# Optimization experiments

Measured on AMD Instinct MI355X. Metric: run time of the kernel, lower is better.

Reference implementation:

```python
import jax, jax.numpy as jnp
import numpy as np
from jax import lax

N = 32768      # total nodes (8 graphs x 4096)
E = 262144     # edges (avg degree 8)
B = 8          # graphs in batch
TW = 25        # time window
H = 128        # hidden features
L = 6          # GNN layers
NV = 1         # n_variables (pos_t only)
SD = 1         # spatial dim
TMAX, TMIN, RES_T = 4.0, 0.0, 250.0
BD_LOW, BD_UP = 0.0, 16.0
EPS = 1e-5


def swish(x):
    return x * jax.nn.sigmoid(x)


def setup_inputs() -> dict:
    key = jax.random.key(0)
    ks = jax.random.split(key, 32)
    s = 0.05
    u = jax.random.normal(ks[0], (N, TW), jnp.float32)
    pos_t = jax.random.uniform(ks[1], (N, 1), jnp.float32) * TMAX
    pos_x = jax.random.uniform(ks[2], (N, 1), jnp.float32) * BD_UP
    pos = jnp.concatenate([pos_t, pos_x], axis=-1)
    edge_index = jax.random.randint(ks[3], (2, E), 0, N, jnp.int64)
    batch = jnp.repeat(jnp.arange(B, dtype=jnp.int64), N // B)
    d_in = TW + SD + NV          # 27
    d_msg = 2 * H + TW + SD + NV  # 282
    d_upd = H + H + NV            # 257
    We1 = jax.random.normal(ks[4], (d_in, H), jnp.float32) * s
    be1 = jnp.zeros((H,), jnp.float32)
    We2 = jax.random.normal(ks[5], (H, H), jnp.float32) * s
    be2 = jnp.zeros((H,), jnp.float32)
    Wm1 = jax.random.normal(ks[6], (L, d_msg, H), jnp.float32) * s
    bm1 = jnp.zeros((L, H), jnp.float32)
    Wm2 = jax.random.normal(ks[7], (L, H, H), jnp.float32) * s
    bm2 = jnp.zeros((L, H), jnp.float32)
    Wu1 = jax.random.normal(ks[8], (L, d_upd, H), jnp.float32) * s
    bu1 = jnp.zeros((L, H), jnp.float32)
    Wu2 = jax.random.normal(ks[9], (L, H, H), jnp.float32) * s
    bu2 = jnp.zeros((L, H), jnp.float32)
    Wc1 = jax.random.normal(ks[10], (8, 1, 16), jnp.float32) * s  # OIH
    bc1 = jnp.zeros((8,), jnp.float32)
    Wc2 = jax.random.normal(ks[11], (1, 8, 14), jnp.float32) * s
    bc2 = jnp.zeros((1,), jnp.float32)
    return dict(u=u, pos=pos, edge_index=edge_index, batch=batch,
                We1=We1, be1=be1, We2=We2, be2=be2,
                Wm1=Wm1, bm1=bm1, Wm2=Wm2, bm2=bm2,
                Wu1=Wu1, bu1=bu1, Wu2=Wu2, bu2=bu2,
                Wc1=Wc1, bc1=bc1, Wc2=Wc2, bc2=bc2)


def _mpnn(u, pos, edge_index, batch, We1, be1, We2, be2,
          Wm1, bm1, Wm2, bm2, Wu1, bu1, Wu2, bu2, Wc1, bc1, Wc2, bc2):
    src = edge_index[0]   # j (source)
    tgt = edge_index[1]   # i (target)
    pos_t = pos[:, 0:1] / TMAX
    pos_x = (pos[:, 1:] - BD_LOW) / (BD_UP - BD_LOW)
    variables = pos_t  # eq_variables empty -> only normalized time

    node_input = jnp.concatenate([u, pos_x, variables], axis=-1)  # [N, 27]
    h = swish(node_input @ We1 + be1)
    h = swish(h @ We2 + be2)

    # in-degree for scatter-mean (empty targets -> 0 like PyG mean)
    cnt = jnp.zeros((N,), jnp.float32).at[tgt].add(1.0)
    cnt = jnp.maximum(cnt, 1.0)[:, None]
    # per-graph node counts for InstanceNorm
    gcnt = jax.ops.segment_sum(jnp.ones((N,), jnp.float32), batch, num_segments=B)[:, None]

    u_diff_e = u[tgt] - u[src]          # [E, TW]
    p_diff_e = pos_x[tgt] - pos_x[src]  # [E, SD]
    var_i_e = variables[tgt]            # [E, NV]

    for l in range(L):
        # message: gather -> MLP per edge
        m_in = jnp.concatenate([h[tgt], h[src], u_diff_e, p_diff_e, var_i_e], axis=-1)  # [E, 282]
        msg = swish(m_in @ Wm1[l] + bm1[l])
        msg = swish(msg @ Wm2[l] + bm2[l])
        # scatter-mean aggregate onto targets
        agg = jax.ops.segment_sum(msg, tgt, num_segments=N) / cnt  # [N, H]
        # node update MLP, residual (in_features == out_features)
        up = jnp.concatenate([h, agg, variables], axis=-1)  # [N, 257]
        up = swish(up @ Wu1[l] + bu1[l])
        up = swish(up @ Wu2[l] + bu2[l])
        h = h + up
        # InstanceNorm per graph (no affine), biased variance
        mean = jax.ops.segment_sum(h, batch, num_segments=B) / gcnt      # [B, H]
        sq = jax.ops.segment_sum(h * h, batch, num_segments=B) / gcnt    # [B, H]
        var = sq - mean * mean
        h = (h - mean[batch]) / jnp.sqrt(var[batch] + EPS)

    # output CNN: tw=25 branch
    hc = h[:, None, :]  # [N, 1, 128]
    dn = ('NCH', 'OIH', 'NCH')
    c = lax.conv_general_dilated(hc, Wc1, (3,), 'VALID', dimension_numbers=dn) + bc1[None, :, None]
    c = swish(c)
    c = lax.conv_general_dilated(c, Wc2, (1,), 'VALID', dimension_numbers=dn) + bc2[None, :, None]
    diff = c[:, 0, :]  # [N, 25]

    dt = (TMAX - TMIN) / RES_T
    dt_cum = jnp.arange(1, TW + 1, dtype=jnp.float32) * dt  # cumsum of ones*dt
    out = u[:, -1:] + dt_cum[None, :] * diff
    return out


def reference(u, pos, edge_index, batch, We1, be1, We2, be2,
              Wm1, bm1, Wm2, bm2, Wu1, bu1, Wu2, bu2, Wc1, bc1, Wc2, bc2):
    return _mpnn(u, pos, edge_index, batch, We1, be1, We2, be2,
                 Wm1, bm1, Wm2, bm2, Wu1, bu1, Wu2, bu2, Wc1, bc1, Wc2, bc2)
```

## Files before the change

kernel.cpp:

```cpp
#include <hip/hip_runtime.h>
#include <stdint.h>

#define N_NODES 32768
#define N_EDGES 262144
#define NB 8
#define TW 25

typedef __attribute__((ext_vector_type(8))) short short8;
typedef __attribute__((ext_vector_type(4))) float floatx4;

#if defined(__has_builtin)
#if __has_builtin(__builtin_amdgcn_cvt_pk_bf16_f32)
#define HAVE_CVT_PK_BF16 1
#endif
#endif

__device__ __forceinline__ float swishf(float x) {
    return x * __builtin_amdgcn_rcpf(1.0f + __expf(-x));
}

__device__ __forceinline__ unsigned short f2bf(float x) {
    union { float f; unsigned u; } v; v.f = x;
    unsigned r = v.u + 0x7FFFu + ((v.u >> 16) & 1u);
    return (unsigned short)(r >> 16);
}
__device__ __forceinline__ unsigned pkbf(float a, float b) {
#ifdef HAVE_CVT_PK_BF16
    typedef __attribute__((ext_vector_type(2))) __bf16 bf16x2;
    union { bf16x2 v; unsigned u; } cv;
    cv.v = __builtin_amdgcn_cvt_pk_bf16_f32(a, b);
    return cv.u;
#else
    return (unsigned)f2bf(a) | ((unsigned)f2bf(b) << 16);
#endif
}
__device__ __forceinline__ float bf2f(unsigned short b) {
    union { unsigned u; float f; } v; v.u = ((unsigned)b) << 16; return v.f;
}

__global__ void init_kernel(const float* __restrict__ pos, const float* __restrict__ u,
                            float* __restrict__ posx, float* __restrict__ post,
                            unsigned short* __restrict__ feat) {
    int i = blockIdx.x * 256 + threadIdx.x;
    if (i < N_NODES) {
        float pt = pos[i * 2 + 0] * 0.25f;
        float px = pos[i * 2 + 1] * 0.0625f;
        post[i] = pt;
        posx[i] = px;
        unsigned short f[32];
        #pragma unroll
        for (int k = 0; k < 25; ++k) f[k] = f2bf(u[(size_t)i * 25 + k]);
        f[25] = f2bf(px);
        f[26] = f2bf(pt);
        #pragma unroll
        for (int k = 27; k < 32; ++k) f[k] = 0;
        #pragma unroll
        for (int j = 0; j < 4; ++j)
            *(uint4*)(feat + (size_t)i * 32 + j * 8) = *(uint4*)&f[j * 8];
    }
}

__global__ void deg_kernel(const int* __restrict__ tgt, int* __restrict__ deg) {
    int i = blockIdx.x * 256 + threadIdx.x;
    if (i < N_EDGES) atomicAdd(&deg[tgt[i]], 1);
}

__global__ __launch_bounds__(1024) void scan_kernel(const int* __restrict__ deg,
                                                    int* __restrict__ cursor) {
    __shared__ int ps[1024];
    int t = threadIdx.x;
    int base = t * 32;
    int tot = 0;
    for (int i = 0; i < 32; ++i) tot += deg[base + i];
    ps[t] = tot;
    __syncthreads();
    for (int off = 1; off < 1024; off <<= 1) {
        int v = (t >= off) ? ps[t - off] : 0;
        __syncthreads();
        ps[t] += v;
        __syncthreads();
    }
    int run = ps[t] - tot;
    for (int i = 0; i < 32; ++i) {
        cursor[base + i] = run;
        run += deg[base + i];
    }
}

__global__ void scatter_kernel(const int* __restrict__ src, const int* __restrict__ tgt,
                               int* __restrict__ cursor,
                               int* __restrict__ src_s, int* __restrict__ tgt_s) {
    int i = blockIdx.x * 256 + threadIdx.x;
    if (i < N_EDGES) {
        int tg = tgt[i];
        int p = atomicAdd(&cursor[tg], 1);
        src_s[p] = src[i];
        tgt_s[p] = tg;
    }
}

__global__ __launch_bounds__(256) void pack_kernel(const float* __restrict__ W,
                                                   unsigned short* __restrict__ Wp,
                                                   int Kreal, int Kc, int total) {
    int id = blockIdx.x * 256 + threadIdx.x;
    if (id >= total) return;
    int lane = id & 63;
    int t8 = (id >> 6) & 7;
    int rest = id >> 9;
    int c = rest % Kc;
    int l = rest / Kc;
    int n = t8 * 16 + (lane & 15);
    int kb = c * 32 + (lane >> 4) * 8;
    short8 v;
    #pragma unroll
    for (int j = 0; j < 8; ++j) {
        int k = kb + j;
        float x = (k < Kreal) ? W[((size_t)l * Kreal + k) * 128 + n] : 0.f;
        v[j] = (short)f2bf(x);
    }
    *(short8*)(Wp + (size_t)id * 8) = v;
}

__global__ __launch_bounds__(256) void pack_cat_kernel(const float* __restrict__ Wm1,
                                                       unsigned short* __restrict__ Wp) {
    int id = blockIdx.x * 256 + threadIdx.x;
    if (id >= 30720) return;
    int lane = id & 63;
    int tile = (id >> 6) & 15;
    int rest = id >> 10;
    int c = rest % 5;
    int l = rest / 5;
    int n = tile * 16 + (lane & 15);
    int col = n & 127;
    bool isT = n < 128;
    int kb = c * 32 + (lane >> 4) * 8;
    const float* W = Wm1 + (size_t)l * 283 * 128;
    short8 v;
    #pragma unroll
    for (int j = 0; j < 8; ++j) {
        int k = kb + j;
        float x = 0.f;
        if (k < 128) {
            x = W[(size_t)(isT ? k : 128 + k) * 128 + col];
        } else if (k < 155) {
            int row = 256 + (k - 128);
            x = W[(size_t)row * 128 + col];
            if (!isT) x = (row == 282) ? 0.f : -x;
        }
        v[j] = (short)f2bf(x);
    }
    *(short8*)(Wp + (size_t)id * 8) = v;
}

__global__ __launch_bounds__(256) void encoder_kernel(
    const float* __restrict__ u, const float* __restrict__ posx,
    const float* __restrict__ post,
    const float* __restrict__ We1, const float* __restrict__ be1,
    const float* __restrict__ We2, const float* __restrict__ be2,
    unsigned short* __restrict__ hraw, float* __restrict__ agg)
{
    __shared__ __align__(16) float As_[64 * 36];
    __shared__ __align__(16) float Ws[32 * 128];
    __shared__ __align__(16) float Ms[64 * 128];

    int t = threadIdx.x;
    int n0 = blockIdx.x * 64;
    int rg = t >> 5, cg = t & 31;

    {
        int r = t & 63, cseg = t >> 6;
        float4 z = make_float4(0.f, 0.f, 0.f, 0.f);
        #pragma unroll
        for (int j = 0; j < 8; ++j)
            *(float4*)(agg + (size_t)(n0 + r) * 128 + cseg * 32 + j * 4) = z;
    }

    float acc[8][4] = {};
    {
        int kk = t >> 3, cb = (t & 7) * 16;
        #pragma unroll
        for (int j = 0; j < 4; ++j) {
            float4 w = make_float4(0.f, 0.f, 0.f, 0.f);
            if (kk < 27) w = *(const float4*)&We1[kk * 128 + cb + j * 4];
            *(float4*)&Ws[kk * 128 + cb + j * 4] = w;
        }
        int el = t >> 2, kb = (t & 3) * 8, n = n0 + el;
        float v[8];
        #pragma unroll
        for (int j = 0; j < 8; ++j) {
            int k = kb + j;
            float x = 0.f;
            if (k < 25) x = u[n * 25 + k];
            else if (k == 25) x = posx[n];
            else if (k == 26) x = post[n];
            v[j] = x;
        }
        #pragma unroll
        for (int j = 0; j < 8; j += 4)
            *(float4*)&As_[el * 36 + kb + j] = make_float4(v[j], v[j+1], v[j+2], v[j+3]);
        __syncthreads();
        #pragma unroll 4
        for (int kk2 = 0; kk2 < 32; ++kk2) {
            float4 b = *(const float4*)&Ws[kk2 * 128 + cg * 4];
            float a[8];
            #pragma unroll
            for (int i = 0; i < 8; ++i) a[i] = As_[(rg * 8 + i) * 36 + kk2];
            #pragma unroll
            for (int i = 0; i < 8; ++i) {
                acc[i][0] += a[i] * b.x; acc[i][1] += a[i] * b.y;
                acc[i][2] += a[i] * b.z; acc[i][3] += a[i] * b.w;
            }
        }
        __syncthreads();
    }
    {
        float4 b1 = *(const float4*)&be1[cg * 4];
        #pragma unroll
        for (int i = 0; i < 8; ++i) {
            float4 m;
            m.x = swishf(acc[i][0] + b1.x);
            m.y = swishf(acc[i][1] + b1.y);
            m.z = swishf(acc[i][2] + b1.z);
            m.w = swishf(acc[i][3] + b1.w);
            *(float4*)&Ms[(rg * 8 + i) * 128 + cg * 4] = m;
        }
        __syncthreads();
    }
    float acc2[8][4] = {};
    for (int k0 = 0; k0 < 128; k0 += 32) {
        int kk = t >> 3, cb = (t & 7) * 16;
        #pragma unroll
        for (int j = 0; j < 4; ++j)
            *(float4*)&Ws[kk * 128 + cb + j * 4] =
                *(const float4*)&We2[(k0 + kk) * 128 + cb + j * 4];
        __syncthreads();
        #pragma unroll 4
        for (int kk2 = 0; kk2 < 32; ++kk2) {
            float4 b = *(const float4*)&Ws[kk2 * 128 + cg * 4];
            float a[8];
            #pragma unroll
            for (int i = 0; i < 8; ++i) a[i] = Ms[(rg * 8 + i) * 128 + (k0 + kk2)];
            #pragma unroll
            for (int i = 0; i < 8; ++i) {
                acc2[i][0] += a[i] * b.x; acc2[i][1] += a[i] * b.y;
                acc2[i][2] += a[i] * b.z; acc2[i][3] += a[i] * b.w;
            }
        }
        __syncthreads();
    }
    {
        float4 b2 = *(const float4*)&be2[cg * 4];
        #pragma unroll
        for (int i = 0; i < 8; ++i) {
            int n = n0 + rg * 8 + i;
            float4 o;
            o.x = swishf(acc2[i][0] + b2.x);
            o.y = swishf(acc2[i][1] + b2.y);
            o.z = swishf(acc2[i][2] + b2.z);
            o.w = swishf(acc2[i][3] + b2.w);
            uint2 pk;
            pk.x = pkbf(o.x, o.y);
            pk.y = pkbf(o.z, o.w);
            *(uint2*)(hraw + (size_t)n * 128 + cg * 4) = pk;
        }
    }
}

__global__ __launch_bounds__(512, 4) void premsg_kernel(
    const unsigned short* __restrict__ hraw,
    const float* __restrict__ stats, int donorm,
    const unsigned short* __restrict__ feat,
    const unsigned short* __restrict__ Wp, const float* __restrict__ b1,
    unsigned short* __restrict__ h_bf,
    float* __restrict__ At, float* __restrict__ As)
{
    __shared__ __align__(16) unsigned short A[64 * 168];
    __shared__ float mean_s[128];
    __shared__ float rstd_s[128];

    int t = threadIdx.x;
    int n0 = blockIdx.x * 64;
    int bidx = n0 >> 12;

    if (t < 128) {
        float mn = 0.f, rs = 1.f;
        if (donorm) {
            float s1 = stats[bidx * 128 + t] * (1.f / 4096.f);
            float s2 = stats[(NB + bidx) * 128 + t] * (1.f / 4096.f);
            mn = s1;
            rs = rsqrtf(s2 - s1 * s1 + 1e-5f);
        }
        mean_s[t] = mn;
        rstd_s[t] = rs;
    }
    __syncthreads();

    {
        int r = t & 63, cseg = t >> 6;
        int n = n0 + r;
        uint4 raw0 = *(const uint4*)(hraw + (size_t)n * 128 + cseg * 16);
        uint4 raw1 = *(const uint4*)(hraw + (size_t)n * 128 + cseg * 16 + 8);
        unsigned pk[8];
        #pragma unroll
        for (int j = 0; j < 8; ++j) {
            unsigned word = (j < 4) ? ((const unsigned*)&raw0)[j]
                                    : ((const unsigned*)&raw1)[j - 4];
            int c0 = cseg * 16 + j * 2;
            float v0 = (bf2f((unsigned short)(word & 0xffffu)) - mean_s[c0]) * rstd_s[c0];
            float v1 = (bf2f((unsigned short)(word >> 16)) - mean_s[c0 + 1]) * rstd_s[c0 + 1];
            pk[j] = pkbf(v0, v1);
        }
        *(uint4*)(A + r * 168 + cseg * 16)     = *(uint4*)&pk[0];
        *(uint4*)(A + r * 168 + cseg * 16 + 8) = *(uint4*)&pk[4];
        *(uint4*)(h_bf + (size_t)n * 128 + cseg * 16)     = *(uint4*)&pk[0];
        *(uint4*)(h_bf + (size_t)n * 128 + cseg * 16 + 8) = *(uint4*)&pk[4];
        if (cseg < 2) {
            uint4 f0 = *(const uint4*)(feat + (size_t)n * 32 + cseg * 16);
            uint4 f1 = *(const uint4*)(feat + (size_t)n * 32 + cseg * 16 + 8);
            *(uint4*)(A + r * 168 + 128 + cseg * 16)     = f0;
            *(uint4*)(A + r * 168 + 128 + cseg * 16 + 8) = f1;
        }
    }
    __syncthreads();

    int w = t >> 6, lane = t & 63, q = lane >> 4, m = lane & 15;
    floatx4 accT[4] = {};
    floatx4 accS[4] = {};
    #pragma unroll
    for (int c = 0; c < 5; ++c) {
        short8 bT = *(const short8*)(Wp + ((size_t)(c * 16 + w) * 64 + lane) * 8);
        short8 bS = *(const short8*)(Wp + ((size_t)(c * 16 + 8 + w) * 64 + lane) * 8);
        #pragma unroll
        for (int g2 = 0; g2 < 4; ++g2) {
            short8 a = *(const short8*)(A + (g2 * 16 + m) * 168 + c * 32 + q * 8);
            accT[g2] = __builtin_amdgcn_mfma_f32_16x16x32_bf16(a, bT, accT[g2], 0, 0, 0);
            accS[g2] = __builtin_amdgcn_mfma_f32_16x16x32_bf16(a, bS, accS[g2], 0, 0, 0);
        }
    }
    int col = w * 16 + m;
    float bv = b1[col];
    #pragma unroll
    for (int g2 = 0; g2 < 4; ++g2) {
        #pragma unroll
        for (int r = 0; r < 4; ++r) {
            int row = g2 * 16 + q * 4 + r;
            At[(size_t)(n0 + row) * 128 + col] = accT[g2][r] + bv;
            As[(size_t)(n0 + row) * 128 + col] = accS[g2][r];
        }
    }
}

__global__ __launch_bounds__(512, 8) void message_kernel(
    const float* __restrict__ At, const float* __restrict__ As,
    const int* __restrict__ src_s, const int* __restrict__ tgt_s,
    const unsigned short* __restrict__ W2p, const float* __restrict__ b2,
    float* __restrict__ agg, float* __restrict__ stats)
{
    __shared__ __align__(16) unsigned short Msh[64 * 136];
    __shared__ __align__(16) unsigned short Cs[64 * 132];
    __shared__ int tgtS[64];

    int t = threadIdx.x;
    int e0 = blockIdx.x * 64;
    if (blockIdx.x == 0 && t < 256) {
        float4 z = make_float4(0.f, 0.f, 0.f, 0.f);
        *(float4*)&stats[t * 8] = z;
        *(float4*)&stats[t * 8 + 4] = z;
    }
    if (t < 64) tgtS[t] = tgt_s[e0 + t];

    {
        int r = t & 63, cseg = t >> 6;
        int g = tgt_s[e0 + r], s = src_s[e0 + r];
        const float4* at = (const float4*)(At + (size_t)g * 128 + cseg * 16);
        const float4* as = (const float4*)(As + (size_t)s * 128 + cseg * 16);
        unsigned pk[8];
        #pragma unroll
        for (int j = 0; j < 4; ++j) {
            float4 a = at[j], bb = as[j];
            pk[2 * j]     = pkbf(swishf(a.x + bb.x), swishf(a.y + bb.y));
            pk[2 * j + 1] = pkbf(swishf(a.z + bb.z), swishf(a.w + bb.w));
        }
        *(uint4*)(Msh + r * 136 + cseg * 16)     = *(uint4*)&pk[0];
        *(uint4*)(Msh + r * 136 + cseg * 16 + 8) = *(uint4*)&pk[4];
    }
    __syncthreads();

    int w = t >> 6, lane = t & 63, q = lane >> 4, m = lane & 15;

    floatx4 acc2[4] = {};
    #pragma unroll
    for (int c = 0; c < 4; ++c) {
        short8 b = *(const short8*)(W2p + ((size_t)(c * 8 + w) * 64 + lane) * 8);
        #pragma unroll
        for (int g2 = 0; g2 < 4; ++g2) {
            short8 a = *(const short8*)(Msh + (g2 * 16 + m) * 136 + c * 32 + q * 8);
            acc2[g2] = __builtin_amdgcn_mfma_f32_16x16x32_bf16(a, b, acc2[g2], 0, 0, 0);
        }
    }
    {
        int col = w * 16 + m;
        float bv = b2[col];
        #pragma unroll
        for (int g2 = 0; g2 < 4; ++g2) {
            unsigned p01 = pkbf(swishf(acc2[g2][0] + bv), swishf(acc2[g2][1] + bv));
            unsigned p23 = pkbf(swishf(acc2[g2][2] + bv), swishf(acc2[g2][3] + bv));
            int base = g2 * 16 + q * 4;
            Cs[(base + 0) * 132 + col] = (unsigned short)p01;
            Cs[(base + 1) * 132 + col] = (unsigned short)(p01 >> 16);
            Cs[(base + 2) * 132 + col] = (unsigned short)p23;
            Cs[(base + 3) * 132 + col] = (unsigned short)(p23 >> 16);
        }
    }
    __syncthreads();

    {
        int col = t & 127, seg = t >> 7;
        int r0 = seg * 16;
        float run = 0.f;
        int prev = tgtS[r0];
        bool atStart = true;
        #pragma unroll 4
        for (int i = 0; i < 16; ++i) {
            int tg = tgtS[r0 + i];
            if (tg != prev) {
                float* dst = &agg[(size_t)prev * 128 + col];
                if (atStart) atomicAdd(dst, run);
                else *dst = run;
                run = 0.f; prev = tg; atStart = false;
            }
            run += bf2f(Cs[(r0 + i) * 132 + col]);
        }
        atomicAdd(&agg[(size_t)prev * 128 + col], run);
    }
}

__global__ __launch_bounds__(512, 4) void update_kernel(
    unsigned short* __restrict__ hraw, const unsigned short* __restrict__ h_bf,
    float* __restrict__ agg, const int* __restrict__ deg,
    const float* __restrict__ post,
    const unsigned short* __restrict__ W1p, const float* __restrict__ b1,
    const unsigned short* __restrict__ W2p, const float* __restrict__ b2,
    float* __restrict__ stats)
{
    __shared__ __align__(16) unsigned short SH[64 * 296 + 64 * 136];
    unsigned short* Msh = SH + 64 * 296;

    int t = threadIdx.x;
    int n0 = blockIdx.x * 64;

    {
        int r = t & 63, cseg = t >> 6;
        int n = n0 + r;
        const short8* hn = (const short8*)(h_bf + (size_t)n * 128);
        #pragma unroll
        for (int j = 0; j < 2; ++j) {
            int chunk = cseg * 2 + j;
            *(short8*)(SH + r * 296 + chunk * 8) = hn[chunk];
        }
        float ic = __builtin_amdgcn_rcpf(fmaxf((float)deg[n], 1.0f));
        #pragma unroll
        for (int j = 0; j < 2; ++j) {
            int unit = cseg * 2 + j;
            const float* ap = agg + (size_t)n * 128 + unit * 8;
            float4 v0 = *(const float4*)ap;
            float4 v1 = *(const float4*)(ap + 4);
            unsigned pa[4];
            pa[0] = pkbf(v0.x * ic, v0.y * ic);
            pa[1] = pkbf(v0.z * ic, v0.w * ic);
            pa[2] = pkbf(v1.x * ic, v1.y * ic);
            pa[3] = pkbf(v1.z * ic, v1.w * ic);
            *(uint4*)(SH + r * 296 + 128 + unit * 8) = *(uint4*)pa;
        }
        if (cseg < 4) {
            short8 z;
            #pragma unroll
            for (int k = 0; k < 8; ++k) z[k] = 0;
            if (cseg == 0) z[0] = (short)f2bf(post[n]);
            *(short8*)(SH + r * 296 + 256 + cseg * 8) = z;
        }
    }
    __syncthreads();

    int w = t >> 6, lane = t & 63, q = lane >> 4, m = lane & 15;

    floatx4 acc[4] = {};
    #pragma unroll
    for (int c = 0; c < 9; ++c) {
        short8 b = *(const short8*)(W1p + ((size_t)(c * 8 + w) * 64 + lane) * 8);
        #pragma unroll
        for (int g2 = 0; g2 < 4; ++g2) {
            short8 a = *(const short8*)(SH + (g2 * 16 + m) * 296 + c * 32 + q * 8);
            acc[g2] = __builtin_amdgcn_mfma_f32_16x16x32_bf16(a, b, acc[g2], 0, 0, 0);
        }
    }
    {
        int col = w * 16 + m;
        float bv = b1[col];
        #pragma unroll
        for (int g2 = 0; g2 < 4; ++g2) {
            unsigned p01 = pkbf(swishf(acc[g2][0] + bv), swishf(acc[g2][1] + bv));
            unsigned p23 = pkbf(swishf(acc[g2][2] + bv), swishf(acc[g2][3] + bv));
            int base = g2 * 16 + q * 4;
            Msh[(base + 0) * 136 + col] = (unsigned short)p01;
            Msh[(base + 1) * 136 + col] = (unsigned short)(p01 >> 16);
            Msh[(base + 2) * 136 + col] = (unsigned short)p23;
            Msh[(base + 3) * 136 + col] = (unsigned short)(p23 >> 16);
        }
    }
    __syncthreads();

    floatx4 acc2[4] = {};
    #pragma unroll
    for (int c = 0; c < 4; ++c) {
        short8 b = *(const short8*)(W2p + ((size_t)(c * 8 + w) * 64 + lane) * 8);
        #pragma unroll
        for (int g2 = 0; g2 < 4; ++g2) {
            short8 a = *(const short8*)(Msh + (g2 * 16 + m) * 136 + c * 32 + q * 8);
            acc2[g2] = __builtin_amdgcn_mfma_f32_16x16x32_bf16(a, b, acc2[g2], 0, 0, 0);
        }
    }

    int bidx = n0 >> 12;
    int col = w * 16 + m;
    float bv = b2[col];
    float s = 0.f, s2 = 0.f;
    #pragma unroll
    for (int g2 = 0; g2 < 4; ++g2) {
        #pragma unroll
        for (int r = 0; r < 4; ++r) {
            int row = g2 * 16 + q * 4 + r;
            float res = bf2f(SH[row * 296 + col]);
            float hv = res + swishf(acc2[g2][r] + bv);
            hraw[(size_t)(n0 + row) * 128 + col] = f2bf(hv);
            s += hv; s2 += hv * hv;
        }
    }
    s  += __shfl_xor(s, 16);  s  += __shfl_xor(s, 32);
    s2 += __shfl_xor(s2, 16); s2 += __shfl_xor(s2, 32);
    if (q == 0) {
        atomicAdd(&stats[bidx * 128 + col], s);
        atomicAdd(&stats[(NB + bidx) * 128 + col], s2);
    }
    {
        int r = t & 63, cseg = t >> 6;
        float4 z = make_float4(0.f, 0.f, 0.f, 0.f);
        #pragma unroll
        for (int j = 0; j < 4; ++j)
            *(float4*)(agg + (size_t)(n0 + r) * 128 + cseg * 16 + j * 4) = z;
    }
}

__global__ __launch_bounds__(256) void conv_kernel(
    const unsigned short* __restrict__ hraw, const float* __restrict__ stats,
    const float* __restrict__ u,
    const float* __restrict__ Wc1, const float* __restrict__ bc1,
    const float* __restrict__ Wc2, const float* __restrict__ bc2,
    float* __restrict__ out)
{
    __shared__ float hs[4][128];
    __shared__ float c1[4][8 * 40];
    int w = threadIdx.x >> 6, lane = threadIdx.x & 63;
    int n = blockIdx.x * 4 + w;
    int b = n >> 12;
    #pragma unroll
    for (int h2 = 0; h2 < 2; ++h2) {
        int c = lane + h2 * 64;
        float s1 = stats[b * 128 + c] * (1.f / 4096.f);
        float s2 = stats[(NB + b) * 128 + c] * (1.f / 4096.f);
        float rs = rsqrtf(s2 - s1 * s1 + 1e-5f);
        hs[w][c] = (bf2f(hraw[(size_t)n * 128 + c]) - s1) * rs;
    }
    __syncthreads();
    for (int idx = lane; idx < 304; idx += 64) {
        int o = idx / 38, p = idx % 38;
        float s = bc1[o];
        #pragma unroll
        for (int k = 0; k < 16; ++k) s += hs[w][p * 3 + k] * Wc1[o * 16 + k];
        c1[w][o * 40 + p] = swishf(s);
    }
    __syncthreads();
    if (lane < TW) {
        float s = bc2[0];
        #pragma unroll
        for (int o = 0; o < 8; ++o)
            for (int k = 0; k < 14; ++k)
                s += c1[w][o * 40 + lane + k] * Wc2[o * 14 + k];
        float dt_cum = (float)(lane + 1) * (4.0f / 250.0f);
        out[n * TW + lane] = u[n * 25 + 24] + dt_cum * s;
    }
}

extern "C" void kernel_launch(void* const* d_in, const int* in_sizes, int n_in,
                              void* d_out, int out_size, void* d_ws, size_t ws_size,
                              hipStream_t stream)
{
    const float* u   = (const float*)d_in[0];
    const float* pos = (const float*)d_in[1];
    const int*   ei  = (const int*)d_in[2];
    const float* We1 = (const float*)d_in[4];
    const float* be1 = (const float*)d_in[5];
    const float* We2 = (const float*)d_in[6];
    const float* be2 = (const float*)d_in[7];
    const float* Wm1 = (const float*)d_in[8];
    const float* bm1 = (const float*)d_in[9];
    const float* Wm2 = (const float*)d_in[10];
    const float* bm2 = (const float*)d_in[11];
    const float* Wu1 = (const float*)d_in[12];
    const float* bu1 = (const float*)d_in[13];
    const float* Wu2 = (const float*)d_in[14];
    const float* bu2 = (const float*)d_in[15];
    const float* Wc1 = (const float*)d_in[16];
    const float* bc1 = (const float*)d_in[17];
    const float* Wc2 = (const float*)d_in[18];
    const float* bc2 = (const float*)d_in[19];
    float* out = (float*)d_out;

    char* base = (char*)d_ws;
    size_t off = 0;
    auto alloc = [&](size_t bytes) -> char* {
        char* r = base + off;
        off = (off + bytes + 511) & ~(size_t)511;
        return r;
    };
    unsigned short* hraw   = (unsigned short*)alloc((size_t)N_NODES * 128 * 2);
    unsigned short* h_bf   = (unsigned short*)alloc((size_t)N_NODES * 128 * 2);
    float*          agg    = (float*)alloc((size_t)N_NODES * 128 * 4);
    float*          At     = (float*)alloc((size_t)N_NODES * 128 * 4);
    float*          As     = (float*)alloc((size_t)N_NODES * 128 * 4);
    float*          posx   = (float*)alloc(N_NODES * 4);
    float*          post   = (float*)alloc(N_NODES * 4);
    unsigned short* feat   = (unsigned short*)alloc((size_t)N_NODES * 32 * 2);
    float*          stats  = (float*)alloc(2 * NB * 128 * 4);
    int*            deg    = (int*)alloc(N_NODES * 4);
    int*            cursor = (int*)alloc(N_NODES * 4);
    int*            src_s  = (int*)alloc((size_t)N_EDGES * 4);
    int*            tgt_s  = (int*)alloc((size_t)N_EDGES * 4);
    unsigned short* Wcat1p = (unsigned short*)alloc((size_t)6 * 5 * 16 * 64 * 8 * 2);
    unsigned short* Wm2p   = (unsigned short*)alloc((size_t)6 * 4 * 4096 * 2);
    unsigned short* Wu1p   = (unsigned short*)alloc((size_t)6 * 9 * 4096 * 2);
    unsigned short* Wu2p   = (unsigned short*)alloc((size_t)6 * 4 * 4096 * 2);
    (void)ws_size;

    const int* srcp = ei;
    const int* tgtp = ei + N_EDGES;

    init_kernel<<<N_NODES / 256, 256, 0, stream>>>(pos, u, posx, post, feat);
    hipMemsetAsync(deg, 0, N_NODES * sizeof(int), stream);
    deg_kernel<<<N_EDGES / 256, 256, 0, stream>>>(tgtp, deg);
    scan_kernel<<<1, 1024, 0, stream>>>(deg, cursor);
    scatter_kernel<<<N_EDGES / 256, 256, 0, stream>>>(srcp, tgtp, cursor, src_s, tgt_s);
    encoder_kernel<<<N_NODES / 64, 256, 0, stream>>>(u, posx, post, We1, be1, We2, be2,
                                                     hraw, agg);
    {
        pack_cat_kernel<<<120, 256, 0, stream>>>(Wm1, Wcat1p);
        int tot1 = 6 * 9 * 512;
        int tot2 = 6 * 4 * 512;
        pack_kernel<<<(tot2 + 255) / 256, 256, 0, stream>>>(Wm2, Wm2p, 128, 4, tot2);
        pack_kernel<<<(tot1 + 255) / 256, 256, 0, stream>>>(Wu1, Wu1p, 257, 9, tot1);
        pack_kernel<<<(tot2 + 255) / 256, 256, 0, stream>>>(Wu2, Wu2p, 128, 4, tot2);
    }

    for (int l = 0; l < 6; ++l) {
        premsg_kernel<<<N_NODES / 64, 512, 0, stream>>>(
            hraw, stats, (l > 0) ? 1 : 0, feat,
            Wcat1p + (size_t)l * 5 * 16 * 64 * 8, bm1 + l * 128,
            h_bf, At, As);
        message_kernel<<<N_EDGES / 64, 512, 0, stream>>>(
            At, As, src_s, tgt_s,
            Wm2p + (size_t)l * 4 * 4096, bm2 + l * 128, agg, stats);
        update_kernel<<<N_NODES / 64, 512, 0, stream>>>(
            hraw, h_bf, agg, deg, post,
            Wu1p + (size_t)l * 9 * 4096, bu1 + l * 128,
            Wu2p + (size_t)l * 4 * 4096, bu2 + l * 128, stats);
    }

    conv_kernel<<<N_NODES / 4, 256, 0, stream>>>(hraw, stats, u, Wc1, bc1, Wc2, bc2, out);
}
```

Before: 650.5 us.

## Restructure message kernel so each wave owns 16 edge rows end-to-end

The message kernel now runs with 256 threads. Each wave gathers and activates its own 16 edge rows straight into MFMA A-fragments in registers, which drops the Msh shared-memory staging buffer and one block barrier. Each wave computes all 8 output column tiles for its rows, streaming W2 fragments from global memory, and segment-reduces its own rows with two columns per lane. The cost is more accumulator registers per wave, and W2 is now re-read by every wave instead of being shared across waves.

```diff
diff --git a/kernel.cpp b/kernel.cpp
--- a/kernel.cpp
+++ b/kernel.cpp
@@ -350,88 +350,97 @@
     }
 }
 
-__global__ __launch_bounds__(512, 8) void message_kernel(
+__global__ __launch_bounds__(256, 4) void message_kernel(
     const float* __restrict__ At, const float* __restrict__ As,
     const int* __restrict__ src_s, const int* __restrict__ tgt_s,
     const unsigned short* __restrict__ W2p, const float* __restrict__ b2,
     float* __restrict__ agg, float* __restrict__ stats)
 {
-    __shared__ __align__(16) unsigned short Msh[64 * 136];
     __shared__ __align__(16) unsigned short Cs[64 * 132];
     __shared__ int tgtS[64];
 
     int t = threadIdx.x;
     int e0 = blockIdx.x * 64;
-    if (blockIdx.x == 0 && t < 256) {
+    if (blockIdx.x == 0) {
         float4 z = make_float4(0.f, 0.f, 0.f, 0.f);
         *(float4*)&stats[t * 8] = z;
         *(float4*)&stats[t * 8 + 4] = z;
     }
     if (t < 64) tgtS[t] = tgt_s[e0 + t];
-
-    {
-        int r = t & 63, cseg = t >> 6;
-        int g = tgt_s[e0 + r], s = src_s[e0 + r];
-        const float4* at = (const float4*)(At + (size_t)g * 128 + cseg * 16);
-        const float4* as = (const float4*)(As + (size_t)s * 128 + cseg * 16);
-        unsigned pk[8];
-        #pragma unroll
-        for (int j = 0; j < 4; ++j) {
-            float4 a = at[j], bb = as[j];
-            pk[2 * j]     = pkbf(swishf(a.x + bb.x), swishf(a.y + bb.y));
-            pk[2 * j + 1] = pkbf(swishf(a.z + bb.z), swishf(a.w + bb.w));
-        }
-        *(uint4*)(Msh + r * 136 + cseg * 16)     = *(uint4*)&pk[0];
-        *(uint4*)(Msh + r * 136 + cseg * 16 + 8) = *(uint4*)&pk[4];
-    }
     __syncthreads();
 
     int w = t >> 6, lane = t & 63, q = lane >> 4, m = lane & 15;
-
-    floatx4 acc2[4] = {};
+    int erow = w * 16 + m;
+    int e = e0 + erow;
+    int gg = tgtS[erow];
+    int ss = src_s[e];
+
+    const float* atp = At + (size_t)gg * 128 + q * 8;
+    const float* asp = As + (size_t)ss * 128 + q * 8;
+    float4 va[8], vb[8];
     #pragma unroll
     for (int c = 0; c < 4; ++c) {
-        short8 b = *(const short8*)(W2p + ((size_t)(c * 8 + w) * 64 + lane) * 8);
-        #pragma unroll
-        for (int g2 = 0; g2 < 4; ++g2) {
-            short8 a = *(const short8*)(Msh + (g2 * 16 + m) * 136 + c * 32 + q * 8);
-            acc2[g2] = __builtin_amdgcn_mfma_f32_16x16x32_bf16(a, b, acc2[g2], 0, 0, 0);
-        }
-    }
-    {
-        int col = w * 16 + m;
-        float bv = b2[col];
-        #pragma unroll
-        for (int g2 = 0; g2 < 4; ++g2) {
-            unsigned p01 = pkbf(swishf(acc2[g2][0] + bv), swishf(acc2[g2][1] + bv));
-            unsigned p23 = pkbf(swishf(acc2[g2][2] + bv), swishf(acc2[g2][3] + bv));
-            int base = g2 * 16 + q * 4;
-            Cs[(base + 0) * 132 + col] = (unsigned short)p01;
-            Cs[(base + 1) * 132 + col] = (unsigned short)(p01 >> 16);
-            Cs[(base + 2) * 132 + col] = (unsigned short)p23;
-            Cs[(base + 3) * 132 + col] = (unsigned short)(p23 >> 16);
-        }
-    }
-    __syncthreads();
-
-    {
-        int col = t & 127, seg = t >> 7;
-        int r0 = seg * 16;
-        float run = 0.f;
+        va[2 * c]     = *(const float4*)(atp + c * 32);
+        va[2 * c + 1] = *(const float4*)(atp + c * 32 + 4);
+        vb[2 * c]     = *(const float4*)(asp + c * 32);
+        vb[2 * c + 1] = *(const float4*)(asp + c * 32 + 4);
+    }
+    short8 af[4];
+    #pragma unroll
+    for (int c = 0; c < 4; ++c) {
+        float4 a0 = va[2 * c], b0 = vb[2 * c];
+        float4 a1 = va[2 * c + 1], b1 = vb[2 * c + 1];
+        union { unsigned u[4]; short8 s; } pk_;
+        pk_.u[0] = pkbf(swishf(a0.x + b0.x), swishf(a0.y + b0.y));
+        pk_.u[1] = pkbf(swishf(a0.z + b0.z), swishf(a0.w + b0.w));
+        pk_.u[2] = pkbf(swishf(a1.x + b1.x), swishf(a1.y + b1.y));
+        pk_.u[3] = pkbf(swishf(a1.z + b1.z), swishf(a1.w + b1.w));
+        af[c] = pk_.s;
+    }
+
+    floatx4 acc[8] = {};
+    #pragma unroll
+    for (int c = 0; c < 4; ++c) {
+        #pragma unroll
+        for (int t8 = 0; t8 < 8; ++t8) {
+            short8 b = *(const short8*)(W2p + ((size_t)(c * 8 + t8) * 64 + lane) * 8);
+            acc[t8] = __builtin_amdgcn_mfma_f32_16x16x32_bf16(af[c], b, acc[t8], 0, 0, 0);
+        }
+    }
+
+    #pragma unroll
+    for (int t8 = 0; t8 < 8; ++t8) {
+        float bv = b2[t8 * 16 + m];
+        unsigned p01 = pkbf(swishf(acc[t8][0] + bv), swishf(acc[t8][1] + bv));
+        unsigned p23 = pkbf(swishf(acc[t8][2] + bv), swishf(acc[t8][3] + bv));
+        int rb = (w * 16 + q * 4) * 132 + t8 * 16 + m;
+        Cs[rb]           = (unsigned short)p01;
+        Cs[rb + 132]     = (unsigned short)(p01 >> 16);
+        Cs[rb + 2 * 132] = (unsigned short)p23;
+        Cs[rb + 3 * 132] = (unsigned short)(p23 >> 16);
+    }
+
+    {
+        int r0 = w * 16;
+        int col0 = lane;
+        float run0 = 0.f, run1 = 0.f;
         int prev = tgtS[r0];
         bool atStart = true;
         #pragma unroll 4
         for (int i = 0; i < 16; ++i) {
             int tg = tgtS[r0 + i];
             if (tg != prev) {
-                float* dst = &agg[(size_t)prev * 128 + col];
-                if (atStart) atomicAdd(dst, run);
-                else *dst = run;
-                run = 0.f; prev = tg; atStart = false;
+                float* d0 = &agg[(size_t)prev * 128 + col0];
+                if (atStart) { atomicAdd(d0, run0); atomicAdd(d0 + 64, run1); }
+                else         { d0[0] = run0;        d0[64] = run1; }
+                run0 = 0.f; run1 = 0.f; prev = tg; atStart = false;
             }
-            run += bf2f(Cs[(r0 + i) * 132 + col]);
-        }
-        atomicAdd(&agg[(size_t)prev * 128 + col], run);
+            run0 += bf2f(Cs[(r0 + i) * 132 + col0]);
+            run1 += bf2f(Cs[(r0 + i) * 132 + col0 + 64]);
+        }
+        float* d0 = &agg[(size_t)prev * 128 + col0];
+        atomicAdd(d0, run0);
+        atomicAdd(d0 + 64, run1);
     }
 }
 
@@ -666,7 +675,7 @@
             hraw, stats, (l > 0) ? 1 : 0, feat,
             Wcat1p + (size_t)l * 5 * 16 * 64 * 8, bm1 + l * 128,
             h_bf, At, As);
-        message_kernel<<<N_EDGES / 64, 512, 0, stream>>>(
+        message_kernel<<<N_EDGES / 64, 256, 0, stream>>>(
             At, As, src_s, tgt_s,
             Wm2p + (size_t)l * 4 * 4096, bm2 + l * 128, agg, stats);
         update_kernel<<<N_NODES / 64, 512, 0, stream>>>(
```

Result: slower. 721.8 us (+11.0%).
